# Kernel optimization log

Measured on AMD Instinct MI355X. Metric: run time of the kernel, lower is better.

The kernel has to match this reference:

```python
import jax, jax.numpy as jnp
import numpy as np

B, L, D = 8, 2048, 64
NEG = -1e9  # matches torch masked fill value -1000000000.0


def setup_inputs() -> dict:
    key = jax.random.key(0)
    kq, kk, kv = jax.random.split(key, 3)
    return {
        "q": jax.random.normal(kq, (B, L, D), dtype=jnp.float32),
        "k": jax.random.normal(kk, (B, L, D), dtype=jnp.float32),
        "v": jax.random.normal(kv, (B, L, D), dtype=jnp.float32),
    }


def reference(q, k, v):
    d_k = q.shape[-1]
    scale = 1.0 / np.sqrt(d_k).astype(np.float32)
    # [B, Lq, Lk] scores
    scores = jnp.einsum("bqd,bkd->bqk", q, k) * scale
    n = scores.shape[-1]
    i = jnp.arange(n)[:, None]
    j = jnp.arange(n)[None, :]
    # fw_mask: tril(diag=-1) of -1e9 -> strictly-lower entries penalized (attend to self+future)
    fw = scores + jnp.where(j < i, jnp.float32(NEG), jnp.float32(0.0))
    # bw_mask: triu(diag=1) of -1e9 -> strictly-upper entries penalized (attend to past+self)
    bw = scores + jnp.where(j > i, jnp.float32(NEG), jnp.float32(0.0))
    out = jnp.einsum("bqk,bkd->bqd", jax.nn.softmax(fw, axis=-1), v) \
        + jnp.einsum("bqk,bkd->bqd", jax.nn.softmax(bw, axis=-1), v)
    return out
```

## Files before the change

kernel.cpp:

```cpp
#include <hip/hip_runtime.h>


typedef __attribute__((ext_vector_type(8))) short short8;
typedef __attribute__((ext_vector_type(4))) float f32x4;

union Frag {
    short8 s;
    unsigned u[4];
    uint4 u4;
};

#define MFMA16(A, B, C) __builtin_amdgcn_mfma_f32_16x16x32_bf16((A), (B), (C), 0, 0, 0)

static constexpr int BB = 8, LL = 2048, DD = 64;
static constexpr float QSCALE = 0.125f * 1.44269504088896340736f;

__device__ __forceinline__ unsigned pk2(float a, float b) {
    unsigned ua = __builtin_bit_cast(unsigned, a) + 0x8000u;
    unsigned ub = __builtin_bit_cast(unsigned, b) + 0x8000u;
    return __builtin_amdgcn_perm(ub, ua, 0x07060302u);
}

__device__ __forceinline__ unsigned bperm(int addr, unsigned v) {
    return (unsigned)__builtin_amdgcn_ds_bpermute(addr, (int)v);
}

__global__ __launch_bounds__(256)
void prepack_frags(const float* __restrict__ K, const float* __restrict__ V,
                   unsigned* __restrict__ Kf, unsigned* __restrict__ Vf) {
    const int t    = threadIdx.x;
    const int lane = t & 63;
    const int col  = lane & 15;
    const int quad = lane >> 4;
    const int g    = t >> 6;
    if (blockIdx.x < 512) {
        const int b = blockIdx.x >> 6, jblk = blockIdx.x & 63, j0 = jblk << 5;
        const int f = g >> 1, h = g & 1;
        const float* src = K + ((size_t)(b * LL) + j0 + 16 * f + col) * DD + h * 32 + quad * 8;
        float4 a0 = *(const float4*)(src);
        float4 a1 = *(const float4*)(src + 4);
        uint4 o = make_uint4(pk2(a0.x, a0.y), pk2(a0.z, a0.w),
                             pk2(a1.x, a1.y), pk2(a1.z, a1.w));
        *(uint4*)(Kf + (size_t)(b * 64 + jblk) * 1024 + t * 4) = o;
    } else {
        const int idx = blockIdx.x - 512;
        const int b = idx >> 6, jblk = idx & 63, j0 = jblk << 5;
        const float* src = V + ((size_t)(b * LL) + j0 + quad * 8) * DD + 16 * g + col;
        float e[8];
        #pragma unroll
        for (int kk = 0; kk < 8; ++kk) e[kk] = src[(size_t)kk * DD];
        uint4 o = make_uint4(pk2(e[0], e[1]), pk2(e[2], e[3]),
                             pk2(e[4], e[5]), pk2(e[6], e[7]));
        *(uint4*)(Vf + (size_t)(b * 64 + jblk) * 1024 + t * 4) = o;
    }
}

__global__ __launch_bounds__(256, 2)
void attn_v4(const float* __restrict__ Q, const unsigned* __restrict__ Kf,
             const unsigned* __restrict__ Vf, float* __restrict__ O) {
    __shared__ __align__(16) float red[18432];

    const int tid  = threadIdx.x;
    const int w    = tid >> 6;
    const int lane = tid & 63;
    const int col  = lane & 15;
    const int quad = lane >> 4;

    const int b  = blockIdx.x & 7;
    const int i0 = (blockIdx.x >> 3) << 5;

    Frag qf[2][2];
    {
        const float* qr = Q + ((size_t)(b * LL) + i0 + col) * DD + quad * 8;
        #pragma unroll
        for (int qt = 0; qt < 2; ++qt) {
            const float* qp = qr + (size_t)qt * 16 * DD;
            float4 a0 = *(const float4*)(qp + 0);
            float4 a1 = *(const float4*)(qp + 4);
            float4 a2 = *(const float4*)(qp + 32);
            float4 a3 = *(const float4*)(qp + 36);
            qf[qt][0].u[0] = pk2(a0.x * QSCALE, a0.y * QSCALE);
            qf[qt][0].u[1] = pk2(a0.z * QSCALE, a0.w * QSCALE);
            qf[qt][0].u[2] = pk2(a1.x * QSCALE, a1.y * QSCALE);
            qf[qt][0].u[3] = pk2(a1.z * QSCALE, a1.w * QSCALE);
            qf[qt][1].u[0] = pk2(a2.x * QSCALE, a2.y * QSCALE);
            qf[qt][1].u[1] = pk2(a2.z * QSCALE, a2.w * QSCALE);
            qf[qt][1].u[2] = pk2(a3.x * QSCALE, a3.y * QSCALE);
            qf[qt][1].u[3] = pk2(a3.z * QSCALE, a3.w * QSCALE);
        }
    }

    const int kbase = w << 9;
    const unsigned* kp = Kf + (size_t)(b * 64 + (kbase >> 5)) * 1024 + lane * 4;
    const unsigned* vp = Vf + (size_t)(b * 64 + (kbase >> 5)) * 1024 + lane * 4;

    f32x4 zero = {0.f, 0.f, 0.f, 0.f};
    f32x4 ot[2][2][4];
    #pragma unroll
    for (int s = 0; s < 2; ++s)
        #pragma unroll
        for (int qt = 0; qt < 2; ++qt)
            #pragma unroll
            for (int c = 0; c < 4; ++c) ot[s][qt][c] = zero;
    float lsF[2] = {0.f, 0.f}, lsB[2] = {0.f, 0.f};

    const int  bpA = (32 * (quad & 1) + col) << 2;
    const bool hiq = quad >= 2;

    Frag kaA[4], vfA[4], kaB[4], vfB[4];
    #pragma unroll
    for (int g = 0; g < 4; ++g) {
        kaA[g].u4 = *(const uint4*)(kp + g * 256);
        vfA[g].u4 = *(const uint4*)(vp + g * 256);
    }

    auto body = [&](Frag (&ck)[4], Frag (&cv)[4], Frag (&nk)[4], Frag (&nv)[4],
                    const int blk) {
        const int j0 = kbase + (blk << 5);
        const int no = ((blk + 1) & 15) << 10;
        #pragma unroll
        for (int g = 0; g < 4; ++g) {
            nk[g].u4 = *(const uint4*)(kp + no + g * 256);
            nv[g].u4 = *(const uint4*)(vp + no + g * 256);
        }

        f32x4 st00 = zero, st01 = zero, st10 = zero, st11 = zero;
        st00 = MFMA16(ck[0].s, qf[0][0].s, st00);
        st00 = MFMA16(ck[1].s, qf[0][1].s, st00);
        st01 = MFMA16(ck[0].s, qf[1][0].s, st01);
        st01 = MFMA16(ck[1].s, qf[1][1].s, st01);
        st10 = MFMA16(ck[2].s, qf[0][0].s, st10);
        st10 = MFMA16(ck[3].s, qf[0][1].s, st10);
        st11 = MFMA16(ck[2].s, qf[1][0].s, st11);
        st11 = MFMA16(ck[3].s, qf[1][1].s, st11);

        float p0[2][4], p1[2][4];
        #pragma unroll
        for (int r = 0; r < 4; ++r) {
            p0[0][r] = exp2f(st00[r]);
            p0[1][r] = exp2f(st01[r]);
            p1[0][r] = exp2f(st10[r]);
            p1[1][r] = exp2f(st11[r]);
        }

        const bool mixed = (j0 == i0);

        if (j0 >= i0) {
            #pragma unroll
            for (int qt = 0; qt < 2; ++qt) {
                float m0[4], m1[4];
                if (mixed) {
                    const int ig = i0 + 16 * qt + col;
                    #pragma unroll
                    for (int r = 0; r < 4; ++r) {
                        const int jg = j0 + 4 * quad + r;
                        m0[r] = (jg >= ig) ? p0[qt][r] : 0.f;
                        m1[r] = (jg + 16 >= ig) ? p1[qt][r] : 0.f;
                    }
                } else {
                    #pragma unroll
                    for (int r = 0; r < 4; ++r) { m0[r] = p0[qt][r]; m1[r] = p1[qt][r]; }
                }
                lsF[qt] += m0[0] + m0[1] + m0[2] + m0[3] + m1[0] + m1[1] + m1[2] + m1[3];
                unsigned x01 = pk2(m0[0], m0[1]), x23 = pk2(m0[2], m0[3]);
                unsigned y01 = pk2(m1[0], m1[1]), y23 = pk2(m1[2], m1[3]);
                unsigned a0 = bperm(bpA, x01),      a1 = bperm(bpA, x23);
                unsigned a2 = bperm(bpA + 64, x01), a3 = bperm(bpA + 64, x23);
                unsigned b0 = bperm(bpA, y01),      b1 = bperm(bpA, y23);
                unsigned b2 = bperm(bpA + 64, y01), b3 = bperm(bpA + 64, y23);
                Frag pf;
                pf.u[0] = hiq ? b0 : a0;
                pf.u[1] = hiq ? b1 : a1;
                pf.u[2] = hiq ? b2 : a2;
                pf.u[3] = hiq ? b3 : a3;
                #pragma unroll
                for (int c = 0; c < 4; ++c)
                    ot[0][qt][c] = MFMA16(cv[c].s, pf.s, ot[0][qt][c]);
            }
        }
        if (j0 <= i0) {
            #pragma unroll
            for (int qt = 0; qt < 2; ++qt) {
                float m0[4], m1[4];
                if (mixed) {
                    const int ig = i0 + 16 * qt + col;
                    #pragma unroll
                    for (int r = 0; r < 4; ++r) {
                        const int jg = j0 + 4 * quad + r;
                        m0[r] = (jg <= ig) ? p0[qt][r] : 0.f;
                        m1[r] = (jg + 16 <= ig) ? p1[qt][r] : 0.f;
                    }
                } else {
                    #pragma unroll
                    for (int r = 0; r < 4; ++r) { m0[r] = p0[qt][r]; m1[r] = p1[qt][r]; }
                }
                lsB[qt] += m0[0] + m0[1] + m0[2] + m0[3] + m1[0] + m1[1] + m1[2] + m1[3];
                unsigned x01 = pk2(m0[0], m0[1]), x23 = pk2(m0[2], m0[3]);
                unsigned y01 = pk2(m1[0], m1[1]), y23 = pk2(m1[2], m1[3]);
                unsigned a0 = bperm(bpA, x01),      a1 = bperm(bpA, x23);
                unsigned a2 = bperm(bpA + 64, x01), a3 = bperm(bpA + 64, x23);
                unsigned b0 = bperm(bpA, y01),      b1 = bperm(bpA, y23);
                unsigned b2 = bperm(bpA + 64, y01), b3 = bperm(bpA + 64, y23);
                Frag pg;
                pg.u[0] = hiq ? b0 : a0;
                pg.u[1] = hiq ? b1 : a1;
                pg.u[2] = hiq ? b2 : a2;
                pg.u[3] = hiq ? b3 : a3;
                #pragma unroll
                for (int c = 0; c < 4; ++c)
                    ot[1][qt][c] = MFMA16(cv[c].s, pg.s, ot[1][qt][c]);
            }
        }
    };

    for (int it = 0; it < 8; ++it) {
        body(kaA, vfA, kaB, vfB, 2 * it);
        body(kaB, vfB, kaA, vfA, 2 * it + 1);
    }

    #pragma unroll
    for (int s = 0; s < 2; ++s)
        #pragma unroll
        for (int qt = 0; qt < 2; ++qt)
            #pragma unroll
            for (int c = 0; c < 4; ++c)
                *(f32x4*)&red[((w * 2 + s) * 32 + qt * 16 + col) * 68 + 16 * c + 4 * quad] =
                    ot[s][qt][c];
    #pragma unroll
    for (int qt = 0; qt < 2; ++qt) {
        red[17408 + (((w * 2 + 0) * 2 + qt) * 4 + quad) * 16 + col] = lsF[qt];
        red[17408 + (((w * 2 + 1) * 2 + qt) * 4 + quad) * 16 + col] = lsB[qt];
    }
    __syncthreads();

    const int q  = tid >> 4;
    const int d0 = (tid & 15) << 2;
    #pragma unroll
    for (int qh = 0; qh < 2; ++qh) {
        const int qq = qh * 16 + q;
        float lf = 0.f, lb = 0.f;
        #pragma unroll
        for (int w2 = 0; w2 < 4; ++w2)
            #pragma unroll
            for (int qd = 0; qd < 4; ++qd) {
                lf += red[17408 + (((w2 * 2 + 0) * 2 + qh) * 4 + qd) * 16 + q];
                lb += red[17408 + (((w2 * 2 + 1) * 2 + qh) * 4 + qd) * 16 + q];
            }
        f32x4 aF = {0.f, 0.f, 0.f, 0.f}, aB = aF;
        #pragma unroll
        for (int w2 = 0; w2 < 4; ++w2) {
            aF += *(const f32x4*)&red[((w2 * 2 + 0) * 32 + qq) * 68 + d0];
            aB += *(const f32x4*)&red[((w2 * 2 + 1) * 32 + qq) * 68 + d0];
        }
        const float rf = 1.0f / lf;
        const float rb = 1.0f / lb;
        float4 o = {aF[0] * rf + aB[0] * rb, aF[1] * rf + aB[1] * rb,
                    aF[2] * rf + aB[2] * rb, aF[3] * rf + aB[3] * rb};
        *(float4*)(O + ((size_t)(b * LL) + i0 + qq) * DD + d0) = o;
    }
}

__global__ __launch_bounds__(256)
void attn_fused_v1(const float* __restrict__ Q, const float* __restrict__ K,
                   const float* __restrict__ V, float* __restrict__ O) {
    __shared__ unsigned smem[8448];
    const int tid  = threadIdx.x;
    const int w    = tid >> 6;
    const int lane = tid & 63;
    const int col  = lane & 15;
    const int quad = lane >> 4;
    const int b  = blockIdx.x >> 7;
    const int i0 = (blockIdx.x & 127) << 4;
    const float* Qb = Q + (size_t)(b * LL + i0) * DD;
    const float* Kb = K + (size_t)b * LL * DD;
    const float* Vb = V + (size_t)b * LL * DD;
    unsigned* VT = smem + w * 1280;
    unsigned* Pb = smem + 5120 + w * 640;
    Frag qf[2];
    {
        const float* qr = Qb + col * DD + quad * 8;
        float4 a0 = *(const float4*)(qr + 0);
        float4 a1 = *(const float4*)(qr + 4);
        float4 a2 = *(const float4*)(qr + 32);
        float4 a3 = *(const float4*)(qr + 36);
        qf[0].u[0] = pk2(a0.x * QSCALE, a0.y * QSCALE);
        qf[0].u[1] = pk2(a0.z * QSCALE, a0.w * QSCALE);
        qf[0].u[2] = pk2(a1.x * QSCALE, a1.y * QSCALE);
        qf[0].u[3] = pk2(a1.z * QSCALE, a1.w * QSCALE);
        qf[1].u[0] = pk2(a2.x * QSCALE, a2.y * QSCALE);
        qf[1].u[1] = pk2(a2.z * QSCALE, a2.w * QSCALE);
        qf[1].u[2] = pk2(a3.x * QSCALE, a3.y * QSCALE);
        qf[1].u[3] = pk2(a3.z * QSCALE, a3.w * QSCALE);
    }
    Frag ones;
    ones.u[0] = ones.u[1] = ones.u[2] = ones.u[3] = 0x3F803F80u;
    f32x4 zero = {0.f, 0.f, 0.f, 0.f};
    f32x4 ot[2][4];
    f32x4 lacc[2];
    lacc[0] = zero; lacc[1] = zero;
    for (int s = 0; s < 2; ++s)
        for (int c = 0; c < 4; ++c) ot[s][c] = zero;
    const int kbase = w << 9;
    const int dj0   = i0 & ~31;
    for (int blk = 0; blk < 16; ++blk) {
        const int j0 = kbase + (blk << 5);
        Frag ka[2][2];
        for (int f = 0; f < 2; ++f) {
            const float* kr = Kb + (size_t)(j0 + f * 16 + col) * DD + quad * 8;
            float4 c0 = *(const float4*)(kr + 0);
            float4 c1 = *(const float4*)(kr + 4);
            float4 c2 = *(const float4*)(kr + 32);
            float4 c3 = *(const float4*)(kr + 36);
            ka[f][0].u[0] = pk2(c0.x, c0.y);
            ka[f][0].u[1] = pk2(c0.z, c0.w);
            ka[f][0].u[2] = pk2(c1.x, c1.y);
            ka[f][0].u[3] = pk2(c1.z, c1.w);
            ka[f][1].u[0] = pk2(c2.x, c2.y);
            ka[f][1].u[1] = pk2(c2.z, c2.w);
            ka[f][1].u[2] = pk2(c3.x, c3.y);
            ka[f][1].u[3] = pk2(c3.z, c3.w);
        }
        for (int u = 0; u < 4; ++u) {
            const int d0 = u * 16 + quad * 4;
            const float* va = Vb + (size_t)(j0 + 2 * col) * DD + d0;
            float4 x = *(const float4*)(va);
            float4 y = *(const float4*)(va + DD);
            VT[(d0 + 0) * 20 + col] = pk2(x.x, y.x);
            VT[(d0 + 1) * 20 + col] = pk2(x.y, y.y);
            VT[(d0 + 2) * 20 + col] = pk2(x.z, y.z);
            VT[(d0 + 3) * 20 + col] = pk2(x.w, y.w);
        }
        f32x4 st0 = zero, st1 = zero;
        st0 = MFMA16(ka[0][0].s, qf[0].s, st0);
        st0 = MFMA16(ka[0][1].s, qf[1].s, st0);
        st1 = MFMA16(ka[1][0].s, qf[0].s, st1);
        st1 = MFMA16(ka[1][1].s, qf[1].s, st1);
        float p0[4], p1[4];
        for (int r = 0; r < 4; ++r) { p0[r] = exp2f(st0[r]); p1[r] = exp2f(st1[r]); }
        bool doF, doB;
        if (j0 == dj0) {
            const int ig = i0 + col;
            unsigned* prowF = Pb + col * 20 + quad * 2;
            unsigned* prowB = prowF + 320;
            float m0[4], m1[4];
            for (int r = 0; r < 4; ++r) {
                const int jg = j0 + 4 * quad + r;
                m0[r] = (jg >= ig) ? p0[r] : 0.f;
                m1[r] = (jg + 16 >= ig) ? p1[r] : 0.f;
            }
            prowF[0] = pk2(m0[0], m0[1]);
            prowF[1] = pk2(m0[2], m0[3]);
            prowF[8] = pk2(m1[0], m1[1]);
            prowF[9] = pk2(m1[2], m1[3]);
            for (int r = 0; r < 4; ++r) {
                const int jg = j0 + 4 * quad + r;
                m0[r] = (jg <= ig) ? p0[r] : 0.f;
                m1[r] = (jg + 16 <= ig) ? p1[r] : 0.f;
            }
            prowB[0] = pk2(m0[0], m0[1]);
            prowB[1] = pk2(m0[2], m0[3]);
            prowB[8] = pk2(m1[0], m1[1]);
            prowB[9] = pk2(m1[2], m1[3]);
            doF = true; doB = true;
        } else if (j0 < i0) {
            unsigned* prowB = Pb + 320 + col * 20 + quad * 2;
            prowB[0] = pk2(p0[0], p0[1]);
            prowB[1] = pk2(p0[2], p0[3]);
            prowB[8] = pk2(p1[0], p1[1]);
            prowB[9] = pk2(p1[2], p1[3]);
            doF = false; doB = true;
        } else {
            unsigned* prowF = Pb + col * 20 + quad * 2;
            prowF[0] = pk2(p0[0], p0[1]);
            prowF[1] = pk2(p0[2], p0[3]);
            prowF[8] = pk2(p1[0], p1[1]);
            prowF[9] = pk2(p1[2], p1[3]);
            doF = true; doB = false;
        }
        Frag vfr[4];
        for (int c = 0; c < 4; ++c)
            vfr[c].u4 = *(const uint4*)(VT + (16 * c + col) * 20 + quad * 4);
        if (doF) {
            Frag pf; pf.u4 = *(const uint4*)(Pb + col * 20 + quad * 4);
            lacc[0] = MFMA16(ones.s, pf.s, lacc[0]);
            for (int c = 0; c < 4; ++c) ot[0][c] = MFMA16(vfr[c].s, pf.s, ot[0][c]);
        }
        if (doB) {
            Frag pg; pg.u4 = *(const uint4*)(Pb + 320 + col * 20 + quad * 4);
            lacc[1] = MFMA16(ones.s, pg.s, lacc[1]);
            for (int c = 0; c < 4; ++c) ot[1][c] = MFMA16(vfr[c].s, pg.s, ot[1][c]);
        }
    }
    __syncthreads();
    float* red  = (float*)smem;
    float* lred = (float*)(smem + 8192);
    for (int s = 0; s < 2; ++s)
        for (int c = 0; c < 4; ++c)
            for (int r = 0; r < 4; ++r)
                red[((w * 2 + s) * 64 + 16 * c + 4 * quad + r) * 16 + col] = ot[s][c][r];
    if (lane < 16) {
        lred[(w * 2 + 0) * 16 + col] = lacc[0][0];
        lred[(w * 2 + 1) * 16 + col] = lacc[1][0];
    }
    __syncthreads();
    const int ri = tid >> 4;
    const int db = (tid & 15) << 2;
    float lf = 0.f, lb = 0.f;
    for (int w2 = 0; w2 < 4; ++w2) {
        lf += lred[(w2 * 2 + 0) * 16 + ri];
        lb += lred[(w2 * 2 + 1) * 16 + ri];
    }
    const float rf = 1.0f / lf;
    const float rb = 1.0f / lb;
    float acc[4];
    for (int kk = 0; kk < 4; ++kk) {
        float af = 0.f, ab = 0.f;
        for (int w2 = 0; w2 < 4; ++w2) {
            af += red[((w2 * 2 + 0) * 64 + db + kk) * 16 + ri];
            ab += red[((w2 * 2 + 1) * 64 + db + kk) * 16 + ri];
        }
        acc[kk] = af * rf + ab * rb;
    }
    float4 o = {acc[0], acc[1], acc[2], acc[3]};
    *(float4*)(O + (size_t)(b * LL + i0 + ri) * DD + db) = o;
}

extern "C" void kernel_launch(void* const* d_in, const int* in_sizes, int n_in,
                              void* d_out, int out_size, void* d_ws, size_t ws_size,
                              hipStream_t stream) {
    const float* q = (const float*)d_in[0];
    const float* k = (const float*)d_in[1];
    const float* v = (const float*)d_in[2];
    float* o = (float*)d_out;
    (void)in_sizes; (void)n_in; (void)out_size;

    const size_t WS_NEED = (size_t)2 * BB * 64 * 1024 * 4 * sizeof(unsigned);
    if (ws_size >= WS_NEED) {
        unsigned* Kf = (unsigned*)d_ws;
        unsigned* Vf = Kf + (size_t)BB * 64 * 1024;
        prepack_frags<<<dim3(1024), dim3(256), 0, stream>>>(k, v, Kf, Vf);
        attn_v4<<<dim3(512), dim3(256), 0, stream>>>(q, Kf, Vf, o);
    } else {
        attn_fused_v1<<<dim3(BB * (LL / 16)), dim3(256), 0, stream>>>(q, k, v, o);
    }
}
```

Before: 84.36 us.

## Stage K/V prepack through LDS and stop double-buffering V fragments

The prepack kernel now loads K and V rows with coalesced float4 reads into shared memory, converts them to bf16 there, and then emits the MFMA fragment layouts from LDS. Previously V was read with strided scalar loads across separate blocks. The attention kernel no longer prefetches V one block ahead in registers; it loads V for the current block inside the loop body, cutting register pressure, but the load latency is now exposed before the PV MFMAs. It also raises wave priority around the MFMA sequences with s_setprio.

```diff
diff --git a/kernel.cpp b/kernel.cpp
--- a/kernel.cpp
+++ b/kernel.cpp
@@ -26,37 +26,57 @@
 }
 
 __global__ __launch_bounds__(256)
-void prepack_frags(const float* __restrict__ K, const float* __restrict__ V,
-                   unsigned* __restrict__ Kf, unsigned* __restrict__ Vf) {
-    const int t    = threadIdx.x;
-    const int lane = t & 63;
-    const int col  = lane & 15;
-    const int quad = lane >> 4;
-    const int g    = t >> 6;
-    if (blockIdx.x < 512) {
-        const int b = blockIdx.x >> 6, jblk = blockIdx.x & 63, j0 = jblk << 5;
+void prepack_v2(const float* __restrict__ K, const float* __restrict__ V,
+                unsigned* __restrict__ Kf, unsigned* __restrict__ Vf) {
+    __shared__ unsigned lk[32 * 36];
+    __shared__ unsigned lv[32 * 36];
+
+    const int t  = threadIdx.x;
+    const int bx = blockIdx.x;
+    const int b = bx >> 6, jblk = bx & 63;
+    const size_t base = ((size_t)(b * LL) + (jblk << 5)) * DD;
+
+    const float4* K4 = (const float4*)(K + base);
+    const float4* V4 = (const float4*)(V + base);
+    #pragma unroll
+    for (int rep = 0; rep < 2; ++rep) {
+        const int m   = t + rep * 256;
+        const float4 x = K4[m];
+        const float4 y = V4[m];
+        const int row = m >> 4;
+        const int cu  = (m & 15) * 2;
+        unsigned* dk = &lk[row * 36 + cu];
+        dk[0] = pk2(x.x, x.y);
+        dk[1] = pk2(x.z, x.w);
+        unsigned* dv = &lv[row * 36 + cu];
+        dv[0] = pk2(y.x, y.y);
+        dv[1] = pk2(y.z, y.w);
+    }
+    __syncthreads();
+
+    const int lane = t & 63, col = lane & 15, quad = lane >> 4, g = t >> 6;
+
+    {
         const int f = g >> 1, h = g & 1;
-        const float* src = K + ((size_t)(b * LL) + j0 + 16 * f + col) * DD + h * 32 + quad * 8;
-        float4 a0 = *(const float4*)(src);
-        float4 a1 = *(const float4*)(src + 4);
-        uint4 o = make_uint4(pk2(a0.x, a0.y), pk2(a0.z, a0.w),
-                             pk2(a1.x, a1.y), pk2(a1.z, a1.w));
-        *(uint4*)(Kf + (size_t)(b * 64 + jblk) * 1024 + t * 4) = o;
-    } else {
-        const int idx = blockIdx.x - 512;
-        const int b = idx >> 6, jblk = idx & 63, j0 = jblk << 5;
-        const float* src = V + ((size_t)(b * LL) + j0 + quad * 8) * DD + 16 * g + col;
-        float e[8];
-        #pragma unroll
-        for (int kk = 0; kk < 8; ++kk) e[kk] = src[(size_t)kk * DD];
-        uint4 o = make_uint4(pk2(e[0], e[1]), pk2(e[2], e[3]),
-                             pk2(e[4], e[5]), pk2(e[6], e[7]));
-        *(uint4*)(Vf + (size_t)(b * 64 + jblk) * 1024 + t * 4) = o;
+        const uint4 o = *(const uint4*)&lk[(16 * f + col) * 36 + 16 * h + 4 * quad];
+        *(uint4*)(Kf + (size_t)bx * 1024 + t * 4) = o;
+    }
+    {
+        unsigned r[8];
+        const int cu = (16 * g + col) >> 1;
+        #pragma unroll
+        for (int k2 = 0; k2 < 8; ++k2) r[k2] = lv[(8 * quad + k2) * 36 + cu];
+        const unsigned sel = (col & 1) ? 0x07060302u : 0x05040100u;
+        const uint4 o = make_uint4(__builtin_amdgcn_perm(r[1], r[0], sel),
+                                   __builtin_amdgcn_perm(r[3], r[2], sel),
+                                   __builtin_amdgcn_perm(r[5], r[4], sel),
+                                   __builtin_amdgcn_perm(r[7], r[6], sel));
+        *(uint4*)(Vf + (size_t)bx * 1024 + t * 4) = o;
     }
 }
 
 __global__ __launch_bounds__(256, 2)
-void attn_v4(const float* __restrict__ Q, const unsigned* __restrict__ Kf,
+void attn_v5(const float* __restrict__ Q, const unsigned* __restrict__ Kf,
              const unsigned* __restrict__ Vf, float* __restrict__ O) {
     __shared__ __align__(16) float red[18432];
 
@@ -107,24 +127,22 @@
     const int  bpA = (32 * (quad & 1) + col) << 2;
     const bool hiq = quad >= 2;
 
-    Frag kaA[4], vfA[4], kaB[4], vfB[4];
-    #pragma unroll
-    for (int g = 0; g < 4; ++g) {
-        kaA[g].u4 = *(const uint4*)(kp + g * 256);
-        vfA[g].u4 = *(const uint4*)(vp + g * 256);
-    }
-
-    auto body = [&](Frag (&ck)[4], Frag (&cv)[4], Frag (&nk)[4], Frag (&nv)[4],
-                    const int blk) {
-        const int j0 = kbase + (blk << 5);
-        const int no = ((blk + 1) & 15) << 10;
-        #pragma unroll
-        for (int g = 0; g < 4; ++g) {
-            nk[g].u4 = *(const uint4*)(kp + no + g * 256);
-            nv[g].u4 = *(const uint4*)(vp + no + g * 256);
-        }
+    Frag kaA[4], kaB[4];
+    #pragma unroll
+    for (int g = 0; g < 4; ++g) kaA[g].u4 = *(const uint4*)(kp + g * 256);
+
+    auto body = [&](Frag (&ck)[4], Frag (&nk)[4], const int blk) {
+        const int j0  = kbase + (blk << 5);
+        const int cur = blk << 10;
+        const int nxt = ((blk + 1) & 15) << 10;
+        #pragma unroll
+        for (int g = 0; g < 4; ++g) nk[g].u4 = *(const uint4*)(kp + nxt + g * 256);
+        Frag cv[4];
+        #pragma unroll
+        for (int g = 0; g < 4; ++g) cv[g].u4 = *(const uint4*)(vp + cur + g * 256);
 
         f32x4 st00 = zero, st01 = zero, st10 = zero, st11 = zero;
+        __builtin_amdgcn_s_setprio(1);
         st00 = MFMA16(ck[0].s, qf[0][0].s, st00);
         st00 = MFMA16(ck[1].s, qf[0][1].s, st00);
         st01 = MFMA16(ck[0].s, qf[1][0].s, st01);
@@ -133,6 +151,7 @@
         st10 = MFMA16(ck[3].s, qf[0][1].s, st10);
         st11 = MFMA16(ck[2].s, qf[1][0].s, st11);
         st11 = MFMA16(ck[3].s, qf[1][1].s, st11);
+        __builtin_amdgcn_s_setprio(0);
 
         float p0[2][4], p1[2][4];
         #pragma unroll
@@ -173,9 +192,11 @@
                 pf.u[1] = hiq ? b1 : a1;
                 pf.u[2] = hiq ? b2 : a2;
                 pf.u[3] = hiq ? b3 : a3;
+                __builtin_amdgcn_s_setprio(1);
                 #pragma unroll
                 for (int c = 0; c < 4; ++c)
                     ot[0][qt][c] = MFMA16(cv[c].s, pf.s, ot[0][qt][c]);
+                __builtin_amdgcn_s_setprio(0);
             }
         }
         if (j0 <= i0) {
@@ -206,16 +227,18 @@
                 pg.u[1] = hiq ? b1 : a1;
                 pg.u[2] = hiq ? b2 : a2;
                 pg.u[3] = hiq ? b3 : a3;
+                __builtin_amdgcn_s_setprio(1);
                 #pragma unroll
                 for (int c = 0; c < 4; ++c)
                     ot[1][qt][c] = MFMA16(cv[c].s, pg.s, ot[1][qt][c]);
+                __builtin_amdgcn_s_setprio(0);
             }
         }
     };
 
     for (int it = 0; it < 8; ++it) {
-        body(kaA, vfA, kaB, vfB, 2 * it);
-        body(kaB, vfB, kaA, vfA, 2 * it + 1);
+        body(kaA, kaB, 2 * it);
+        body(kaB, kaA, 2 * it + 1);
     }
 
     #pragma unroll
@@ -438,8 +461,8 @@
     if (ws_size >= WS_NEED) {
         unsigned* Kf = (unsigned*)d_ws;
         unsigned* Vf = Kf + (size_t)BB * 64 * 1024;
-        prepack_frags<<<dim3(1024), dim3(256), 0, stream>>>(k, v, Kf, Vf);
-        attn_v4<<<dim3(512), dim3(256), 0, stream>>>(q, Kf, Vf, o);
+        prepack_v2<<<dim3(512), dim3(256), 0, stream>>>(k, v, Kf, Vf);
+        attn_v5<<<dim3(512), dim3(256), 0, stream>>>(q, Kf, Vf, o);
     } else {
         attn_fused_v1<<<dim3(BB * (LL / 16)), dim3(256), 0, stream>>>(q, k, v, o);
     }
```

Result: no change. 83.71 us (median of 2 runs) (-0.8%).
